# Optimization experiments

Hardware: AMD Instinct MI355X
Metric: run time of the kernel (lower is better)

The kernel has to match this reference:

```python
import jax, jax.numpy as jnp
import numpy as np

N_TOKENS = 65536   # number of embeddings to quantize
CODE_DIM = 768     # embedding dim
NUM_CODES = 4096   # codebook size


def setup_inputs() -> dict:
    key = jax.random.key(0)
    k1, k2 = jax.random.split(key)
    x = jax.random.normal(k1, (N_TOKENS, CODE_DIM), dtype=jnp.float32)
    codebook = jax.random.normal(k2, (NUM_CODES, CODE_DIM), dtype=jnp.float32)
    return {"x": x, "codebook": codebook}


def reference(x, codebook):
    # argmin over squared distances == argmin over cdist (sqrt is monotone).
    x2 = jnp.sum(x * x, axis=-1, keepdims=True)          # [N, 1]
    c2 = jnp.sum(codebook * codebook, axis=-1)           # [K]
    dist = x2 + c2[None, :] - 2.0 * jnp.einsum('nd,kd->nk', x, codebook)  # [N, K]
    indices = jnp.argmin(dist, axis=-1)                  # [N] int
    quantized = codebook[indices]                        # gather [N, D]
    # straight-through estimator: forward = quantized, grad flows to x
    q_ste = x + jax.lax.stop_gradient(quantized - x)
    return q_ste, indices
```

## Files before the change

kernel.cpp:

```cpp
#include <hip/hip_runtime.h>

#define N_TOKENS  65536
#define CODE_DIM  768
#define NUM_CODES 4096

#define MARGIN 0.006f
#define FLTMAX 3.4028235e38f

typedef __attribute__((ext_vector_type(8))) short bf16x8;
typedef __attribute__((ext_vector_type(4))) float f32x4;

__device__ __forceinline__ unsigned short f2bf(float f) {
  unsigned int u = __float_as_uint(f);
  unsigned int r = (u + 0x7fffu + ((u >> 16) & 1u)) >> 16;
  return (unsigned short)r;
}
__device__ __forceinline__ float bf2f(unsigned short h) {
  return __uint_as_float(((unsigned int)h) << 16);
}
__device__ __forceinline__ void gl2lds16(const void* g, void* l) {
  __builtin_amdgcn_global_load_lds(
      (const __attribute__((address_space(1))) unsigned int*)g,
      (__attribute__((address_space(3))) unsigned int*)l, 16, 0, 0);
}

__global__ __launch_bounds__(256) void vq_convert_kernel(
    const float* __restrict__ x, const float* __restrict__ cb,
    unsigned short* __restrict__ xh, unsigned short* __restrict__ xl,
    unsigned short* __restrict__ cbh, unsigned short* __restrict__ cbl,
    float* __restrict__ x2, float* __restrict__ c2, int* __restrict__ fcnt) {
  if (blockIdx.x == 0 && threadIdx.x == 0) *fcnt = 0;
  const int wave = threadIdx.x >> 6;
  const int lane = threadIdx.x & 63;
  const int row  = blockIdx.x * 4 + wave;
  const float* src;
  unsigned short *hdst, *ldst;
  float* ndst;
  if (row < N_TOKENS) {
    src = x + (size_t)row * CODE_DIM;
    hdst = xh + (size_t)row * CODE_DIM;
    ldst = xl + (size_t)row * CODE_DIM;
    ndst = x2 + row;
  } else {
    const int r = row - N_TOKENS;
    if (r >= NUM_CODES) return;
    src = cb + (size_t)r * CODE_DIM;
    hdst = cbh + (size_t)r * CODE_DIM;
    ldst = cbl + (size_t)r * CODE_DIM;
    ndst = c2 + r;
  }
  const float4* s4 = (const float4*)src;
  ushort4* h4 = (ushort4*)hdst;
  ushort4* l4 = (ushort4*)ldst;
  float acc = 0.f;
#pragma unroll
  for (int i = 0; i < 3; ++i) {
    float4 f = s4[lane + 64 * i];
    ushort4 h, l;
    h.x = f2bf(f.x); l.x = f2bf(f.x - bf2f(h.x));
    h.y = f2bf(f.y); l.y = f2bf(f.y - bf2f(h.y));
    h.z = f2bf(f.z); l.z = f2bf(f.z - bf2f(h.z));
    h.w = f2bf(f.w); l.w = f2bf(f.w - bf2f(h.w));
    h4[lane + 64 * i] = h;
    l4[lane + 64 * i] = l;
    acc += (f.x * f.x + f.y * f.y) + (f.z * f.z + f.w * f.w);
  }
#pragma unroll
  for (int off = 32; off > 0; off >>= 1) acc += __shfl_down(acc, off, 64);
  if (lane == 0) *ndst = acc;
}

#define BT 256
#define KTILE 256
#define NKT (NUM_CODES / KTILE)
#define NSTEP (CODE_DIM / 32)
#define TOTSTEP (NKT * NSTEP)

__global__ __launch_bounds__(512, 2) void vq_mfma_kernel(
    const unsigned short* __restrict__ xh, const unsigned short* __restrict__ xl,
    const unsigned short* __restrict__ cbh, const unsigned short* __restrict__ cbl,
    const float* __restrict__ c2, int* __restrict__ out_idx,
    int* __restrict__ fcnt, int* __restrict__ flist) {
  __shared__ __align__(16) unsigned short sA[2][BT * 64];
  __shared__ __align__(16) unsigned short sB[2][KTILE * 64];
  __shared__ float redv[512], redsv[512];
  __shared__ int   redi[512];

  const int tid = threadIdx.x;
  const int wave = tid >> 6, lane = tid & 63;
  const int l15 = lane & 15, quad = lane >> 4;
  const int wr = wave >> 1, wc = wave & 1;
  const int tokBase = blockIdx.x * BT;

  const int lr = lane >> 3;
  const int cc = (lane & 7) ^ lr;
  const int hsel = cc >> 2;
  const int coff = (cc & 3) * 8;
  const unsigned short* pAsrc = hsel ? xl : xh;
  const unsigned short* pBsrc = hsel ? cbl : cbh;
  const size_t aOff = (size_t)(tokBase + wave * 32 + lr) * CODE_DIM + coff;
  const size_t bOff = (size_t)(wave * 32 + lr) * CODE_DIM + coff;

  const int aposh = (quad ^ (l15 & 7)) * 8;
  const int aBaseH = (wr * 64 + l15) * 64 + aposh;
  const int aBaseL = (wr * 64 + l15) * 64 + (aposh ^ 32);
  const int bBaseH = (wc * 128 + l15) * 64 + aposh;
  const int bBaseL = (wc * 128 + l15) * 64 + (aposh ^ 32);

  float v[4][4], sv[4][4];
  int bi[4][4];
#pragma unroll
  for (int i = 0; i < 4; ++i)
#pragma unroll
    for (int r = 0; r < 4; ++r) { v[i][r] = FLTMAX; sv[i][r] = FLTMAX; bi[i][r] = 0; }

  auto STAGE = [&](int slot, int s) {
    const int sk0 = (s % NSTEP) * 32;
    const size_t sbb = (size_t)(s / NSTEP) * (KTILE * (size_t)CODE_DIM);
#pragma unroll
    for (int t = 0; t < 4; ++t)
      gl2lds16(pAsrc + aOff + (size_t)t * (8 * CODE_DIM) + sk0,
               &sA[slot][(wave * 32 + t * 8) * 64]);
#pragma unroll
    for (int t = 0; t < 4; ++t)
      gl2lds16(pBsrc + sbb + bOff + (size_t)t * (8 * CODE_DIM) + sk0,
               &sB[slot][(wave * 32 + t * 8) * 64]);
  };

  STAGE(0, 0);
  asm volatile("s_waitcnt vmcnt(0)" ::: "memory");
  __builtin_amdgcn_s_barrier();
  __builtin_amdgcn_sched_barrier(0);

  for (int kt = 0; kt < NKT; ++kt) {
    f32x4 acc[4][8];
#pragma unroll
    for (int i = 0; i < 4; ++i)
#pragma unroll
      for (int j = 0; j < 8; ++j) acc[i][j] = (f32x4){0.f, 0.f, 0.f, 0.f};

    for (int ksq = 0; ksq < NSTEP; ++ksq) {
      const int gstep = kt * NSTEP + ksq;
      const int cur = gstep & 1;
      const bool more = (gstep < TOTSTEP - 1);
      if (more) STAGE(cur ^ 1, gstep + 1);

      const unsigned short* As = sA[cur];
      const unsigned short* Bs = sB[cur];
      bf16x8 fah[4], fal[4];
#pragma unroll
      for (int i = 0; i < 4; ++i) {
        fah[i] = *(const bf16x8*)(As + aBaseH + i * 1024);
        fal[i] = *(const bf16x8*)(As + aBaseL + i * 1024);
      }
#pragma unroll
      for (int jp = 0; jp < 4; ++jp) {
        bf16x8 fbh[2], fbl[2];
#pragma unroll
        for (int jj = 0; jj < 2; ++jj) {
          const int j = jp * 2 + jj;
          fbh[jj] = *(const bf16x8*)(Bs + bBaseH + j * 1024);
          fbl[jj] = *(const bf16x8*)(Bs + bBaseL + j * 1024);
        }
        __builtin_amdgcn_s_setprio(1);
#pragma unroll
        for (int i = 0; i < 4; ++i)
#pragma unroll
          for (int jj = 0; jj < 2; ++jj) {
            const int j = jp * 2 + jj;
            acc[i][j] = __builtin_amdgcn_mfma_f32_16x16x32_bf16(fah[i], fbh[jj], acc[i][j], 0, 0, 0);
            acc[i][j] = __builtin_amdgcn_mfma_f32_16x16x32_bf16(fah[i], fbl[jj], acc[i][j], 0, 0, 0);
            acc[i][j] = __builtin_amdgcn_mfma_f32_16x16x32_bf16(fal[i], fbh[jj], acc[i][j], 0, 0, 0);
          }
        __builtin_amdgcn_s_setprio(0);
      }
      asm volatile("s_waitcnt vmcnt(0)" ::: "memory");
      __builtin_amdgcn_s_barrier();
      __builtin_amdgcn_sched_barrier(0);
    }

    const int kbase = kt * KTILE;
#pragma unroll
    for (int j = 0; j < 8; ++j) {
      const int kcol = kbase + wc * 128 + j * 16 + l15;
      const float c2j = c2[kcol];
#pragma unroll
      for (int i = 0; i < 4; ++i)
#pragma unroll
        for (int r = 0; r < 4; ++r) {
          float s = fmaf(-2.0f, acc[i][j][r], c2j);
          float vo = v[i][r];
          sv[i][r] = fminf(sv[i][r], fmaxf(s, vo));
          bool lt = s < vo;
          v[i][r]  = lt ? s : vo;
          bi[i][r] = lt ? kcol : bi[i][r];
        }
    }
  }

#pragma unroll
  for (int i = 0; i < 4; ++i)
#pragma unroll
    for (int r = 0; r < 4; ++r) {
      float vv = v[i][r], svv = sv[i][r];
      int ii = bi[i][r];
#pragma unroll
      for (int m = 1; m < 16; m <<= 1) {
        float ov = __shfl_xor(vv, m, 64);
        float osv = __shfl_xor(svv, m, 64);
        int oi = __shfl_xor(ii, m, 64);
        float nsv = fminf(fminf(svv, osv), fmaxf(vv, ov));
        bool take = (ov < vv) || (ov == vv && oi < ii);
        vv = take ? ov : vv;
        ii = take ? oi : ii;
        svv = nsv;
      }
      if (l15 == 0) {
        int row = wr * 64 + i * 16 + quad * 4 + r;
        redv[row * 2 + wc] = vv;
        redsv[row * 2 + wc] = svv;
        redi[row * 2 + wc] = ii;
      }
    }
  __syncthreads();
  if (tid < 256) {
    float v0 = redv[tid * 2], v1 = redv[tid * 2 + 1];
    float s0 = redsv[tid * 2], s1 = redsv[tid * 2 + 1];
    int i0 = redi[tid * 2], i1 = redi[tid * 2 + 1];
    bool take = (v1 < v0) || (v1 == v0 && i1 < i0);
    float bv = take ? v1 : v0;
    int bidx = take ? i1 : i0;
    float bsv = fminf(fminf(s0, s1), fmaxf(v0, v1));
    out_idx[tokBase + tid] = bidx;
    if (bsv - bv < MARGIN) {
      int p = atomicAdd(fcnt, 1);
      flist[p] = tokBase + tid;
    }
  }
}

__global__ __launch_bounds__(256) void vq_rescan_kernel(
    const float* __restrict__ x, const float* __restrict__ cb,
    const float* __restrict__ x2, const float* __restrict__ c2,
    const int* __restrict__ fcnt, const int* __restrict__ flist,
    int* __restrict__ out_idx) {
  __shared__ float xs[4][CODE_DIM];
  __shared__ float rv[256];
  __shared__ int ri[256];
  const int nf = *fcnt;
  const int ngr = (nf + 3) >> 2;
  for (int g = blockIdx.x; g < ngr; g += gridDim.x) {
    const int base = g * 4;
    int tok[4];
#pragma unroll
    for (int t = 0; t < 4; ++t) tok[t] = flist[min(base + t, nf - 1)];
    __syncthreads();
    if (threadIdx.x < 192) {
#pragma unroll
      for (int t = 0; t < 4; ++t)
        ((float4*)xs[t])[threadIdx.x] =
            ((const float4*)(x + (size_t)tok[t] * CODE_DIM))[threadIdx.x];
    }
    __syncthreads();
    float bv[4]; int bidx[4];
#pragma unroll
    for (int t = 0; t < 4; ++t) { bv[t] = FLTMAX; bidx[t] = 0; }
    for (int kk = 0; kk < NUM_CODES / 256; ++kk) {
      const int k = kk * 256 + threadIdx.x;
      const float4* crow = (const float4*)(cb + (size_t)k * CODE_DIM);
      float a0 = 0.f, a1 = 0.f, a2 = 0.f, a3 = 0.f;
      for (int c = 0; c < CODE_DIM / 4; ++c) {
        float4 cv = crow[c];
        float4 x0 = ((float4*)xs[0])[c];
        float4 x1 = ((float4*)xs[1])[c];
        float4 x2v = ((float4*)xs[2])[c];
        float4 x3 = ((float4*)xs[3])[c];
        a0 += (x0.x * cv.x + x0.y * cv.y) + (x0.z * cv.z + x0.w * cv.w);
        a1 += (x1.x * cv.x + x1.y * cv.y) + (x1.z * cv.z + x1.w * cv.w);
        a2 += (x2v.x * cv.x + x2v.y * cv.y) + (x2v.z * cv.z + x2v.w * cv.w);
        a3 += (x3.x * cv.x + x3.y * cv.y) + (x3.z * cv.z + x3.w * cv.w);
      }
      const float c2k = c2[k];
      float d0 = (x2[tok[0]] + c2k) - 2.0f * a0;
      float d1 = (x2[tok[1]] + c2k) - 2.0f * a1;
      float d2 = (x2[tok[2]] + c2k) - 2.0f * a2;
      float d3 = (x2[tok[3]] + c2k) - 2.0f * a3;
      if (d0 < bv[0]) { bv[0] = d0; bidx[0] = k; }
      if (d1 < bv[1]) { bv[1] = d1; bidx[1] = k; }
      if (d2 < bv[2]) { bv[2] = d2; bidx[2] = k; }
      if (d3 < bv[3]) { bv[3] = d3; bidx[3] = k; }
    }
#pragma unroll
    for (int t = 0; t < 4; ++t) {
      __syncthreads();
      rv[threadIdx.x] = bv[t];
      ri[threadIdx.x] = bidx[t];
      __syncthreads();
      for (int s = 128; s > 0; s >>= 1) {
        if (threadIdx.x < s) {
          float ov = rv[threadIdx.x + s];
          int oi = ri[threadIdx.x + s];
          if (ov < rv[threadIdx.x] ||
              (ov == rv[threadIdx.x] && oi < ri[threadIdx.x])) {
            rv[threadIdx.x] = ov;
            ri[threadIdx.x] = oi;
          }
        }
        __syncthreads();
      }
      if (threadIdx.x == 0 && base + t < nf) out_idx[tok[t]] = ri[0];
    }
  }
}

__global__ __launch_bounds__(256) void vq_gather_kernel(
    const float* __restrict__ cb, const int* __restrict__ idx,
    float* __restrict__ out) {
  const int wave = threadIdx.x >> 6;
  const int lane = threadIdx.x & 63;
  const int token = blockIdx.x * 4 + wave;
  const int k = idx[token];
  const float4* src = (const float4*)(cb + (size_t)k * CODE_DIM);
  float4* dst = (float4*)(out + (size_t)token * CODE_DIM);
#pragma unroll
  for (int i = 0; i < 3; ++i) dst[lane + 64 * i] = src[lane + 64 * i];
  if (lane == 0) out[(size_t)N_TOKENS * CODE_DIM + token] = (float)k;
}

#define MT 64
#define KT 128
#define DT 32
#define LDSTRIDE 36

__global__ __launch_bounds__(256) void vq_norms_kernel(
    const float* __restrict__ x, const float* __restrict__ cb,
    float* __restrict__ x2, float* __restrict__ c2) {
  const int wave = threadIdx.x >> 6;
  const int lane = threadIdx.x & 63;
  const int row = blockIdx.x * 4 + wave;
  const float* src;
  float* dst;
  if (row < N_TOKENS) {
    src = x + (size_t)row * CODE_DIM;
    dst = x2 + row;
  } else {
    const int r = row - N_TOKENS;
    if (r >= NUM_CODES) return;
    src = cb + (size_t)r * CODE_DIM;
    dst = c2 + r;
  }
  const float4* s4 = (const float4*)src;
  float acc = 0.f;
#pragma unroll
  for (int i = 0; i < 3; ++i) {
    float4 vv = s4[lane + 64 * i];
    acc += (vv.x * vv.x + vv.y * vv.y) + (vv.z * vv.z + vv.w * vv.w);
  }
#pragma unroll
  for (int off = 32; off > 0; off >>= 1) acc += __shfl_down(acc, off, 64);
  if (lane == 0) *dst = acc;
}

__global__ __launch_bounds__(256) void vq_argmin_kernel(
    const float* __restrict__ x, const float* __restrict__ cb,
    const float* __restrict__ x2, const float* __restrict__ c2,
    int* __restrict__ out_idx) {
  __shared__ float xs[MT * LDSTRIDE];
  __shared__ float cs[KT * LDSTRIDE];
  __shared__ float x2s[MT];
  __shared__ float c2s[KT];
  const int tid = threadIdx.x;
  const int tx = tid & 15;
  const int ty = tid >> 4;
  const int tokBase = blockIdx.x * MT;
  if (tid < MT) x2s[tid] = x2[tokBase + tid];
  float bestv[4];
  int besti[4];
#pragma unroll
  for (int i = 0; i < 4; ++i) { bestv[i] = FLTMAX; besti[i] = 0; }
  const float4* xg = (const float4*)x;
  const float4* cg = (const float4*)cb;
  for (int kt = 0; kt < NUM_CODES / KT; ++kt) {
    const int kBase = kt * KT;
    __syncthreads();
    if (tid < KT) c2s[tid] = c2[kBase + tid];
    float acc[4][8];
#pragma unroll
    for (int i = 0; i < 4; ++i)
#pragma unroll
      for (int j = 0; j < 8; ++j) acc[i][j] = 0.f;
    for (int dc = 0; dc < CODE_DIM / DT; ++dc) {
      __syncthreads();
#pragma unroll
      for (int r = 0; r < 2; ++r) {
        int fidx = tid + 256 * r;
        int row = fidx >> 3, c4 = fidx & 7;
        float4 vv = xg[(size_t)(tokBase + row) * (CODE_DIM / 4) + dc * 8 + c4];
        *(float4*)&xs[row * LDSTRIDE + c4 * 4] = vv;
      }
#pragma unroll
      for (int r = 0; r < 4; ++r) {
        int fidx = tid + 256 * r;
        int row = fidx >> 3, c4 = fidx & 7;
        float4 vv = cg[(size_t)(kBase + row) * (CODE_DIM / 4) + dc * 8 + c4];
        *(float4*)&cs[row * LDSTRIDE + c4 * 4] = vv;
      }
      __syncthreads();
#pragma unroll
      for (int dd = 0; dd < DT / 4; ++dd) {
        float4 xv[4], cv[8];
#pragma unroll
        for (int i = 0; i < 4; ++i)
          xv[i] = *(const float4*)&xs[(ty + 16 * i) * LDSTRIDE + dd * 4];
#pragma unroll
        for (int j = 0; j < 8; ++j)
          cv[j] = *(const float4*)&cs[(tx + 16 * j) * LDSTRIDE + dd * 4];
#pragma unroll
        for (int i = 0; i < 4; ++i)
#pragma unroll
          for (int j = 0; j < 8; ++j)
            acc[i][j] += (xv[i].x * cv[j].x + xv[i].y * cv[j].y) +
                         (xv[i].z * cv[j].z + xv[i].w * cv[j].w);
      }
    }
#pragma unroll
    for (int i = 0; i < 4; ++i) {
      const float xx = x2s[ty + 16 * i];
#pragma unroll
      for (int j = 0; j < 8; ++j) {
        float dist = (xx + c2s[tx + 16 * j]) - 2.0f * acc[i][j];
        int k = kBase + tx + 16 * j;
        if (dist < bestv[i]) { bestv[i] = dist; besti[i] = k; }
      }
    }
  }
  __syncthreads();
  float* rdv = xs;
  int* rdi = (int*)cs;
#pragma unroll
  for (int i = 0; i < 4; ++i) {
    const int m = ty + 16 * i;
    rdv[m * 16 + tx] = bestv[i];
    rdi[m * 16 + tx] = besti[i];
  }
  __syncthreads();
  if (tid < MT) {
    float bv = rdv[tid * 16];
    int bidx = rdi[tid * 16];
#pragma unroll
    for (int t = 1; t < 16; ++t) {
      float vv = rdv[tid * 16 + t];
      int kk = rdi[tid * 16 + t];
      if (vv < bv || (vv == bv && kk < bidx)) { bv = vv; bidx = kk; }
    }
    out_idx[tokBase + tid] = bidx;
  }
}

extern "C" void kernel_launch(void* const* d_in, const int* in_sizes, int n_in,
                              void* d_out, int out_size, void* d_ws, size_t ws_size,
                              hipStream_t stream) {
  (void)in_sizes; (void)n_in; (void)out_size;
  const float* x = (const float*)d_in[0];
  const float* cb = (const float*)d_in[1];
  float* out = (float*)d_out;

  char* w = (char*)d_ws;
  unsigned short* xh = (unsigned short*)w;  w += (size_t)N_TOKENS * CODE_DIM * 2;
  unsigned short* xl = (unsigned short*)w;  w += (size_t)N_TOKENS * CODE_DIM * 2;
  unsigned short* cbh = (unsigned short*)w; w += (size_t)NUM_CODES * CODE_DIM * 2;
  unsigned short* cbl = (unsigned short*)w; w += (size_t)NUM_CODES * CODE_DIM * 2;
  float* x2 = (float*)w;  w += (size_t)N_TOKENS * 4;
  float* c2 = (float*)w;  w += (size_t)NUM_CODES * 4;
  int* idx = (int*)w;     w += (size_t)N_TOKENS * 4;
  int* flist = (int*)w;   w += (size_t)N_TOKENS * 4;
  int* fcnt = (int*)w;    w += 256;
  const size_t need = (size_t)(w - (char*)d_ws);

  if (ws_size >= need) {
    vq_convert_kernel<<<(N_TOKENS + NUM_CODES) / 4, 256, 0, stream>>>(
        x, cb, xh, xl, cbh, cbl, x2, c2, fcnt);
    vq_mfma_kernel<<<N_TOKENS / BT, 512, 0, stream>>>(
        xh, xl, cbh, cbl, c2, idx, fcnt, flist);
    vq_rescan_kernel<<<512, 256, 0, stream>>>(x, cb, x2, c2, fcnt, flist, idx);
    vq_gather_kernel<<<N_TOKENS / 4, 256, 0, stream>>>(cb, idx, out);
  } else {
    float* fx2 = (float*)d_ws;
    float* fc2 = fx2 + N_TOKENS;
    int* fidx = (int*)(fc2 + NUM_CODES);
    vq_norms_kernel<<<(N_TOKENS + NUM_CODES + 3) / 4, 256, 0, stream>>>(x, cb, fx2, fc2);
    vq_argmin_kernel<<<N_TOKENS / MT, 256, 0, stream>>>(x, cb, fx2, fc2, fidx);
    vq_gather_kernel<<<N_TOKENS / 4, 256, 0, stream>>>(cb, fidx, out);
  }
}
```

Measured before the change: 1.818 ms.

## Fuse codebook gather into MFMA kernel and split staging around MFMA phases

The separate gather kernel is removed. The MFMA kernel now writes the quantized rows and float indices for its own tokens at the end, and the rescan kernel rewrites the rows for flagged tokens with the corrected index. The inner loop is also reordered into three MFMA phases (hi*hi, hi*lo, lo*hi), and the A and B global-to-LDS prefetches are issued between phases instead of together at the start. This saves one kernel launch and a full pass re-reading the index array, and aims for better overlap of loads with MFMA, at the cost of more live B fragment registers (fbh and fbl, 8 each).

```diff
diff --git a/kernel.cpp b/kernel.cpp
--- a/kernel.cpp
+++ b/kernel.cpp
@@ -79,12 +79,14 @@
 __global__ __launch_bounds__(512, 2) void vq_mfma_kernel(
     const unsigned short* __restrict__ xh, const unsigned short* __restrict__ xl,
     const unsigned short* __restrict__ cbh, const unsigned short* __restrict__ cbl,
-    const float* __restrict__ c2, int* __restrict__ out_idx,
+    const float* __restrict__ c2, const float* __restrict__ cb,
+    float* __restrict__ out, int* __restrict__ out_idx,
     int* __restrict__ fcnt, int* __restrict__ flist) {
   __shared__ __align__(16) unsigned short sA[2][BT * 64];
   __shared__ __align__(16) unsigned short sB[2][KTILE * 64];
   __shared__ float redv[512], redsv[512];
   __shared__ int   redi[512];
+  __shared__ int   sIdx[256];
 
   const int tid = threadIdx.x;
   const int wave = tid >> 6, lane = tid & 63;
@@ -114,20 +116,16 @@
 #pragma unroll
     for (int r = 0; r < 4; ++r) { v[i][r] = FLTMAX; sv[i][r] = FLTMAX; bi[i][r] = 0; }
 
-  auto STAGE = [&](int slot, int s) {
-    const int sk0 = (s % NSTEP) * 32;
-    const size_t sbb = (size_t)(s / NSTEP) * (KTILE * (size_t)CODE_DIM);
+  {
 #pragma unroll
     for (int t = 0; t < 4; ++t)
-      gl2lds16(pAsrc + aOff + (size_t)t * (8 * CODE_DIM) + sk0,
-               &sA[slot][(wave * 32 + t * 8) * 64]);
+      gl2lds16(pAsrc + aOff + (size_t)t * (8 * CODE_DIM),
+               &sA[0][(wave * 32 + t * 8) * 64]);
 #pragma unroll
     for (int t = 0; t < 4; ++t)
-      gl2lds16(pBsrc + sbb + bOff + (size_t)t * (8 * CODE_DIM) + sk0,
-               &sB[slot][(wave * 32 + t * 8) * 64]);
-  };
-
-  STAGE(0, 0);
+      gl2lds16(pBsrc + bOff + (size_t)t * (8 * CODE_DIM),
+               &sB[0][(wave * 32 + t * 8) * 64]);
+  }
   asm volatile("s_waitcnt vmcnt(0)" ::: "memory");
   __builtin_amdgcn_s_barrier();
   __builtin_amdgcn_sched_barrier(0);
@@ -143,37 +141,59 @@
       const int gstep = kt * NSTEP + ksq;
       const int cur = gstep & 1;
       const bool more = (gstep < TOTSTEP - 1);
-      if (more) STAGE(cur ^ 1, gstep + 1);
-
+      const int ns = gstep + 1;
+      const int nk0 = (ns % NSTEP) * 32;
+      const size_t nbb = (size_t)(ns / NSTEP) * (KTILE * (size_t)CODE_DIM);
       const unsigned short* As = sA[cur];
       const unsigned short* Bs = sB[cur];
-      bf16x8 fah[4], fal[4];
-#pragma unroll
-      for (int i = 0; i < 4; ++i) {
-        fah[i] = *(const bf16x8*)(As + aBaseH + i * 1024);
-        fal[i] = *(const bf16x8*)(As + aBaseL + i * 1024);
-      }
-#pragma unroll
-      for (int jp = 0; jp < 4; ++jp) {
-        bf16x8 fbh[2], fbl[2];
-#pragma unroll
-        for (int jj = 0; jj < 2; ++jj) {
-          const int j = jp * 2 + jj;
-          fbh[jj] = *(const bf16x8*)(Bs + bBaseH + j * 1024);
-          fbl[jj] = *(const bf16x8*)(Bs + bBaseL + j * 1024);
-        }
-        __builtin_amdgcn_s_setprio(1);
-#pragma unroll
-        for (int i = 0; i < 4; ++i)
-#pragma unroll
-          for (int jj = 0; jj < 2; ++jj) {
-            const int j = jp * 2 + jj;
-            acc[i][j] = __builtin_amdgcn_mfma_f32_16x16x32_bf16(fah[i], fbh[jj], acc[i][j], 0, 0, 0);
-            acc[i][j] = __builtin_amdgcn_mfma_f32_16x16x32_bf16(fah[i], fbl[jj], acc[i][j], 0, 0, 0);
-            acc[i][j] = __builtin_amdgcn_mfma_f32_16x16x32_bf16(fal[i], fbh[jj], acc[i][j], 0, 0, 0);
-          }
-        __builtin_amdgcn_s_setprio(0);
-      }
+
+      if (more) {
+#pragma unroll
+        for (int t = 0; t < 4; ++t)
+          gl2lds16(pAsrc + aOff + (size_t)t * (8 * CODE_DIM) + nk0,
+                   &sA[cur ^ 1][(wave * 32 + t * 8) * 64]);
+      }
+
+      bf16x8 fah[4], fal[4], fbh[8], fbl[8];
+#pragma unroll
+      for (int i = 0; i < 4; ++i) fah[i] = *(const bf16x8*)(As + aBaseH + i * 1024);
+#pragma unroll
+      for (int j = 0; j < 8; ++j) fbh[j] = *(const bf16x8*)(Bs + bBaseH + j * 1024);
+      __builtin_amdgcn_s_setprio(1);
+#pragma unroll
+      for (int i = 0; i < 4; ++i)
+#pragma unroll
+        for (int j = 0; j < 8; ++j)
+          acc[i][j] = __builtin_amdgcn_mfma_f32_16x16x32_bf16(fah[i], fbh[j], acc[i][j], 0, 0, 0);
+      __builtin_amdgcn_s_setprio(0);
+
+      if (more) {
+#pragma unroll
+        for (int t = 0; t < 4; ++t)
+          gl2lds16(pBsrc + nbb + bOff + (size_t)t * (8 * CODE_DIM) + nk0,
+                   &sB[cur ^ 1][(wave * 32 + t * 8) * 64]);
+      }
+
+#pragma unroll
+      for (int j = 0; j < 8; ++j) fbl[j] = *(const bf16x8*)(Bs + bBaseL + j * 1024);
+      __builtin_amdgcn_s_setprio(1);
+#pragma unroll
+      for (int i = 0; i < 4; ++i)
+#pragma unroll
+        for (int j = 0; j < 8; ++j)
+          acc[i][j] = __builtin_amdgcn_mfma_f32_16x16x32_bf16(fah[i], fbl[j], acc[i][j], 0, 0, 0);
+      __builtin_amdgcn_s_setprio(0);
+
+#pragma unroll
+      for (int i = 0; i < 4; ++i) fal[i] = *(const bf16x8*)(As + aBaseL + i * 1024);
+      __builtin_amdgcn_s_setprio(1);
+#pragma unroll
+      for (int i = 0; i < 4; ++i)
+#pragma unroll
+        for (int j = 0; j < 8; ++j)
+          acc[i][j] = __builtin_amdgcn_mfma_f32_16x16x32_bf16(fal[i], fbh[j], acc[i][j], 0, 0, 0);
+      __builtin_amdgcn_s_setprio(0);
+
       asm volatile("s_waitcnt vmcnt(0)" ::: "memory");
       __builtin_amdgcn_s_barrier();
       __builtin_amdgcn_sched_barrier(0);
@@ -232,18 +252,30 @@
     int bidx = take ? i1 : i0;
     float bsv = fminf(fminf(s0, s1), fmaxf(v0, v1));
     out_idx[tokBase + tid] = bidx;
+    sIdx[tid] = bidx;
     if (bsv - bv < MARGIN) {
       int p = atomicAdd(fcnt, 1);
       flist[p] = tokBase + tid;
     }
   }
+  __syncthreads();
+  for (int tt = 0; tt < 32; ++tt) {
+    const int t = wave * 32 + tt;
+    const int k = sIdx[t];
+    const float4* src = (const float4*)(cb + (size_t)k * CODE_DIM);
+    float4* dst = (float4*)(out + (size_t)(tokBase + t) * CODE_DIM);
+#pragma unroll
+    for (int i2 = 0; i2 < 3; ++i2) dst[lane + 64 * i2] = src[lane + 64 * i2];
+  }
+  if (tid < 256)
+    out[(size_t)N_TOKENS * CODE_DIM + tokBase + tid] = (float)sIdx[tid];
 }
 
 __global__ __launch_bounds__(256) void vq_rescan_kernel(
     const float* __restrict__ x, const float* __restrict__ cb,
     const float* __restrict__ x2, const float* __restrict__ c2,
     const int* __restrict__ fcnt, const int* __restrict__ flist,
-    int* __restrict__ out_idx) {
+    int* __restrict__ out_idx, float* __restrict__ out) {
   __shared__ float xs[4][CODE_DIM];
   __shared__ float rv[256];
   __shared__ int ri[256];
@@ -308,7 +340,16 @@
         }
         __syncthreads();
       }
-      if (threadIdx.x == 0 && base + t < nf) out_idx[tok[t]] = ri[0];
+      const int kfix = ri[0];
+      if (base + t < nf) {
+        if (threadIdx.x < 192)
+          ((float4*)(out + (size_t)tok[t] * CODE_DIM))[threadIdx.x] =
+              ((const float4*)(cb + (size_t)kfix * CODE_DIM))[threadIdx.x];
+        if (threadIdx.x == 0) {
+          out_idx[tok[t]] = kfix;
+          out[(size_t)N_TOKENS * CODE_DIM + tok[t]] = (float)kfix;
+        }
+      }
     }
   }
 }
@@ -481,9 +522,8 @@
     vq_convert_kernel<<<(N_TOKENS + NUM_CODES) / 4, 256, 0, stream>>>(
         x, cb, xh, xl, cbh, cbl, x2, c2, fcnt);
     vq_mfma_kernel<<<N_TOKENS / BT, 512, 0, stream>>>(
-        xh, xl, cbh, cbl, c2, idx, fcnt, flist);
-    vq_rescan_kernel<<<512, 256, 0, stream>>>(x, cb, x2, c2, fcnt, flist, idx);
-    vq_gather_kernel<<<N_TOKENS / 4, 256, 0, stream>>>(cb, idx, out);
+        xh, xl, cbh, cbl, c2, cb, out, idx, fcnt, flist);
+    vq_rescan_kernel<<<512, 256, 0, stream>>>(x, cb, x2, c2, fcnt, flist, idx, out);
   } else {
     float* fx2 = (float*)d_ws;
     float* fc2 = fx2 + N_TOKENS;
```

Result: slower. 1.934 ms (+6.4%).

## Replace split-bf16 three-pass MFMA with single fp16 MFMA and wider rescan margin

Applied to the files above, without the earlier changes.

Replaces the bf16 hi/lo split (three MFMAs per tile, which emulates fp32) with a single fp16 conversion and one f16 MFMA per K chunk. Each LDS stage now carries 64 K-elements, which cuts both the matrix-core work and the global traffic for the converted operands. Because fp16 is less precise, the ambiguity margin grows from 0.006 to 0.12, so more tokens fall back to the exact fp32 rescan. The rescan kernel is widened to handle 8 tokens per group to absorb that larger fallback list. The risk is that rescan cost grows sharply, and the fixed margin may not cover the fp16 error on every input.

```diff
diff --git a/kernel.cpp b/kernel.cpp
--- a/kernel.cpp
+++ b/kernel.cpp
@@ -4,19 +4,15 @@
 #define CODE_DIM  768
 #define NUM_CODES 4096
 
-#define MARGIN 0.006f
+#define MARGIN 0.12f
 #define FLTMAX 3.4028235e38f
 
-typedef __attribute__((ext_vector_type(8))) short bf16x8;
+typedef __attribute__((ext_vector_type(8))) _Float16 f16x8;
 typedef __attribute__((ext_vector_type(4))) float f32x4;
 
-__device__ __forceinline__ unsigned short f2bf(float f) {
-  unsigned int u = __float_as_uint(f);
-  unsigned int r = (u + 0x7fffu + ((u >> 16) & 1u)) >> 16;
-  return (unsigned short)r;
-}
-__device__ __forceinline__ float bf2f(unsigned short h) {
-  return __uint_as_float(((unsigned int)h) << 16);
+__device__ __forceinline__ unsigned short f2h(float f) {
+  _Float16 h = (_Float16)f;
+  return *(unsigned short*)&h;
 }
 __device__ __forceinline__ void gl2lds16(const void* g, void* l) {
   __builtin_amdgcn_global_load_lds(
@@ -26,43 +22,35 @@
 
 __global__ __launch_bounds__(256) void vq_convert_kernel(
     const float* __restrict__ x, const float* __restrict__ cb,
-    unsigned short* __restrict__ xh, unsigned short* __restrict__ xl,
-    unsigned short* __restrict__ cbh, unsigned short* __restrict__ cbl,
+    unsigned short* __restrict__ xh, unsigned short* __restrict__ ch,
     float* __restrict__ x2, float* __restrict__ c2, int* __restrict__ fcnt) {
   if (blockIdx.x == 0 && threadIdx.x == 0) *fcnt = 0;
   const int wave = threadIdx.x >> 6;
   const int lane = threadIdx.x & 63;
   const int row  = blockIdx.x * 4 + wave;
   const float* src;
-  unsigned short *hdst, *ldst;
+  unsigned short* hdst;
   float* ndst;
   if (row < N_TOKENS) {
     src = x + (size_t)row * CODE_DIM;
     hdst = xh + (size_t)row * CODE_DIM;
-    ldst = xl + (size_t)row * CODE_DIM;
     ndst = x2 + row;
   } else {
     const int r = row - N_TOKENS;
     if (r >= NUM_CODES) return;
     src = cb + (size_t)r * CODE_DIM;
-    hdst = cbh + (size_t)r * CODE_DIM;
-    ldst = cbl + (size_t)r * CODE_DIM;
+    hdst = ch + (size_t)r * CODE_DIM;
     ndst = c2 + r;
   }
   const float4* s4 = (const float4*)src;
   ushort4* h4 = (ushort4*)hdst;
-  ushort4* l4 = (ushort4*)ldst;
   float acc = 0.f;
 #pragma unroll
   for (int i = 0; i < 3; ++i) {
     float4 f = s4[lane + 64 * i];
-    ushort4 h, l;
-    h.x = f2bf(f.x); l.x = f2bf(f.x - bf2f(h.x));
-    h.y = f2bf(f.y); l.y = f2bf(f.y - bf2f(h.y));
-    h.z = f2bf(f.z); l.z = f2bf(f.z - bf2f(h.z));
-    h.w = f2bf(f.w); l.w = f2bf(f.w - bf2f(h.w));
+    ushort4 h;
+    h.x = f2h(f.x); h.y = f2h(f.y); h.z = f2h(f.z); h.w = f2h(f.w);
     h4[lane + 64 * i] = h;
-    l4[lane + 64 * i] = l;
     acc += (f.x * f.x + f.y * f.y) + (f.z * f.z + f.w * f.w);
   }
 #pragma unroll
@@ -73,12 +61,11 @@
 #define BT 256
 #define KTILE 256
 #define NKT (NUM_CODES / KTILE)
-#define NSTEP (CODE_DIM / 32)
-#define TOTSTEP (NKT * NSTEP)
+#define NST (CODE_DIM / 64)
+#define TOT (NKT * NST)
 
 __global__ __launch_bounds__(512, 2) void vq_mfma_kernel(
-    const unsigned short* __restrict__ xh, const unsigned short* __restrict__ xl,
-    const unsigned short* __restrict__ cbh, const unsigned short* __restrict__ cbl,
+    const unsigned short* __restrict__ xh, const unsigned short* __restrict__ ch,
     const float* __restrict__ c2, int* __restrict__ out_idx,
     int* __restrict__ fcnt, int* __restrict__ flist) {
   __shared__ __align__(16) unsigned short sA[2][BT * 64];
@@ -93,19 +80,15 @@
   const int tokBase = blockIdx.x * BT;
 
   const int lr = lane >> 3;
-  const int cc = (lane & 7) ^ lr;
-  const int hsel = cc >> 2;
-  const int coff = (cc & 3) * 8;
-  const unsigned short* pAsrc = hsel ? xl : xh;
-  const unsigned short* pBsrc = hsel ? cbl : cbh;
-  const size_t aOff = (size_t)(tokBase + wave * 32 + lr) * CODE_DIM + coff;
-  const size_t bOff = (size_t)(wave * 32 + lr) * CODE_DIM + coff;
-
-  const int aposh = (quad ^ (l15 & 7)) * 8;
-  const int aBaseH = (wr * 64 + l15) * 64 + aposh;
-  const int aBaseL = (wr * 64 + l15) * 64 + (aposh ^ 32);
-  const int bBaseH = (wc * 128 + l15) * 64 + aposh;
-  const int bBaseL = (wc * 128 + l15) * 64 + (aposh ^ 32);
+  const int cSrc = (lane & 7) ^ lr;
+  const size_t aOff = (size_t)(tokBase + wave * 32 + lr) * CODE_DIM + cSrc * 8;
+  const size_t bOff = (size_t)(wave * 32 + lr) * CODE_DIM + cSrc * 8;
+
+  const int apos = (quad ^ (l15 & 7)) * 8;
+  const int aB0 = (wr * 64 + l15) * 64 + apos;
+  const int aB1 = (wr * 64 + l15) * 64 + (apos ^ 32);
+  const int bB0 = (wc * 128 + l15) * 64 + apos;
+  const int bB1 = (wc * 128 + l15) * 64 + (apos ^ 32);
 
   float v[4][4], sv[4][4];
   int bi[4][4];
@@ -115,15 +98,15 @@
     for (int r = 0; r < 4; ++r) { v[i][r] = FLTMAX; sv[i][r] = FLTMAX; bi[i][r] = 0; }
 
   auto STAGE = [&](int slot, int s) {
-    const int sk0 = (s % NSTEP) * 32;
-    const size_t sbb = (size_t)(s / NSTEP) * (KTILE * (size_t)CODE_DIM);
+    const int kw = (s % NST) * 64;
+    const size_t rb = (size_t)(s / NST) * (KTILE * (size_t)CODE_DIM);
 #pragma unroll
     for (int t = 0; t < 4; ++t)
-      gl2lds16(pAsrc + aOff + (size_t)t * (8 * CODE_DIM) + sk0,
+      gl2lds16(xh + aOff + (size_t)t * (8 * CODE_DIM) + kw,
                &sA[slot][(wave * 32 + t * 8) * 64]);
 #pragma unroll
     for (int t = 0; t < 4; ++t)
-      gl2lds16(pBsrc + sbb + bOff + (size_t)t * (8 * CODE_DIM) + sk0,
+      gl2lds16(ch + rb + bOff + (size_t)t * (8 * CODE_DIM) + kw,
                &sB[slot][(wave * 32 + t * 8) * 64]);
   };
 
@@ -139,41 +122,37 @@
 #pragma unroll
       for (int j = 0; j < 8; ++j) acc[i][j] = (f32x4){0.f, 0.f, 0.f, 0.f};
 
-    for (int ksq = 0; ksq < NSTEP; ++ksq) {
-      const int gstep = kt * NSTEP + ksq;
+    for (int ks = 0; ks < NST; ++ks) {
+      const int gstep = kt * NST + ks;
       const int cur = gstep & 1;
-      const bool more = (gstep < TOTSTEP - 1);
-      if (more) STAGE(cur ^ 1, gstep + 1);
-
       const unsigned short* As = sA[cur];
       const unsigned short* Bs = sB[cur];
-      bf16x8 fah[4], fal[4];
-#pragma unroll
-      for (int i = 0; i < 4; ++i) {
-        fah[i] = *(const bf16x8*)(As + aBaseH + i * 1024);
-        fal[i] = *(const bf16x8*)(As + aBaseL + i * 1024);
-      }
-#pragma unroll
-      for (int jp = 0; jp < 4; ++jp) {
-        bf16x8 fbh[2], fbl[2];
-#pragma unroll
-        for (int jj = 0; jj < 2; ++jj) {
-          const int j = jp * 2 + jj;
-          fbh[jj] = *(const bf16x8*)(Bs + bBaseH + j * 1024);
-          fbl[jj] = *(const bf16x8*)(Bs + bBaseL + j * 1024);
-        }
-        __builtin_amdgcn_s_setprio(1);
-#pragma unroll
-        for (int i = 0; i < 4; ++i)
-#pragma unroll
-          for (int jj = 0; jj < 2; ++jj) {
-            const int j = jp * 2 + jj;
-            acc[i][j] = __builtin_amdgcn_mfma_f32_16x16x32_bf16(fah[i], fbh[jj], acc[i][j], 0, 0, 0);
-            acc[i][j] = __builtin_amdgcn_mfma_f32_16x16x32_bf16(fah[i], fbl[jj], acc[i][j], 0, 0, 0);
-            acc[i][j] = __builtin_amdgcn_mfma_f32_16x16x32_bf16(fal[i], fbh[jj], acc[i][j], 0, 0, 0);
-          }
-        __builtin_amdgcn_s_setprio(0);
-      }
+      if (gstep < TOT - 1) STAGE(cur ^ 1, gstep + 1);
+
+      f16x8 fa[4], fb[8];
+#pragma unroll
+      for (int i = 0; i < 4; ++i) fa[i] = *(const f16x8*)(As + aB0 + i * 1024);
+#pragma unroll
+      for (int j = 0; j < 8; ++j) fb[j] = *(const f16x8*)(Bs + bB0 + j * 1024);
+      __builtin_amdgcn_s_setprio(1);
+#pragma unroll
+      for (int i = 0; i < 4; ++i)
+#pragma unroll
+        for (int j = 0; j < 8; ++j)
+          acc[i][j] = __builtin_amdgcn_mfma_f32_16x16x32_f16(fa[i], fb[j], acc[i][j], 0, 0, 0);
+      __builtin_amdgcn_s_setprio(0);
+#pragma unroll
+      for (int i = 0; i < 4; ++i) fa[i] = *(const f16x8*)(As + aB1 + i * 1024);
+#pragma unroll
+      for (int j = 0; j < 8; ++j) fb[j] = *(const f16x8*)(Bs + bB1 + j * 1024);
+      __builtin_amdgcn_s_setprio(1);
+#pragma unroll
+      for (int i = 0; i < 4; ++i)
+#pragma unroll
+        for (int j = 0; j < 8; ++j)
+          acc[i][j] = __builtin_amdgcn_mfma_f32_16x16x32_f16(fa[i], fb[j], acc[i][j], 0, 0, 0);
+      __builtin_amdgcn_s_setprio(0);
+
       asm volatile("s_waitcnt vmcnt(0)" ::: "memory");
       __builtin_amdgcn_s_barrier();
       __builtin_amdgcn_sched_barrier(0);
@@ -244,54 +223,50 @@
     const float* __restrict__ x2, const float* __restrict__ c2,
     const int* __restrict__ fcnt, const int* __restrict__ flist,
     int* __restrict__ out_idx) {
-  __shared__ float xs[4][CODE_DIM];
+  __shared__ float xs[8][CODE_DIM];
   __shared__ float rv[256];
   __shared__ int ri[256];
   const int nf = *fcnt;
-  const int ngr = (nf + 3) >> 2;
+  const int ngr = (nf + 7) >> 3;
   for (int g = blockIdx.x; g < ngr; g += gridDim.x) {
-    const int base = g * 4;
-    int tok[4];
-#pragma unroll
-    for (int t = 0; t < 4; ++t) tok[t] = flist[min(base + t, nf - 1)];
+    const int base = g * 8;
+    int tok[8];
+#pragma unroll
+    for (int t = 0; t < 8; ++t) tok[t] = flist[min(base + t, nf - 1)];
     __syncthreads();
     if (threadIdx.x < 192) {
 #pragma unroll
-      for (int t = 0; t < 4; ++t)
+      for (int t = 0; t < 8; ++t)
         ((float4*)xs[t])[threadIdx.x] =
             ((const float4*)(x + (size_t)tok[t] * CODE_DIM))[threadIdx.x];
     }
     __syncthreads();
-    float bv[4]; int bidx[4];
-#pragma unroll
-    for (int t = 0; t < 4; ++t) { bv[t] = FLTMAX; bidx[t] = 0; }
+    float bv[8]; int bidx[8];
+#pragma unroll
+    for (int t = 0; t < 8; ++t) { bv[t] = FLTMAX; bidx[t] = 0; }
     for (int kk = 0; kk < NUM_CODES / 256; ++kk) {
       const int k = kk * 256 + threadIdx.x;
       const float4* crow = (const float4*)(cb + (size_t)k * CODE_DIM);
-      float a0 = 0.f, a1 = 0.f, a2 = 0.f, a3 = 0.f;
+      float a[8];
+#pragma unroll
+      for (int t = 0; t < 8; ++t) a[t] = 0.f;
       for (int c = 0; c < CODE_DIM / 4; ++c) {
         float4 cv = crow[c];
-        float4 x0 = ((float4*)xs[0])[c];
-        float4 x1 = ((float4*)xs[1])[c];
-        float4 x2v = ((float4*)xs[2])[c];
-        float4 x3 = ((float4*)xs[3])[c];
-        a0 += (x0.x * cv.x + x0.y * cv.y) + (x0.z * cv.z + x0.w * cv.w);
-        a1 += (x1.x * cv.x + x1.y * cv.y) + (x1.z * cv.z + x1.w * cv.w);
-        a2 += (x2v.x * cv.x + x2v.y * cv.y) + (x2v.z * cv.z + x2v.w * cv.w);
-        a3 += (x3.x * cv.x + x3.y * cv.y) + (x3.z * cv.z + x3.w * cv.w);
+#pragma unroll
+        for (int t = 0; t < 8; ++t) {
+          float4 xv = ((float4*)xs[t])[c];
+          a[t] += (xv.x * cv.x + xv.y * cv.y) + (xv.z * cv.z + xv.w * cv.w);
+        }
       }
       const float c2k = c2[k];
-      float d0 = (x2[tok[0]] + c2k) - 2.0f * a0;
-      float d1 = (x2[tok[1]] + c2k) - 2.0f * a1;
-      float d2 = (x2[tok[2]] + c2k) - 2.0f * a2;
-      float d3 = (x2[tok[3]] + c2k) - 2.0f * a3;
-      if (d0 < bv[0]) { bv[0] = d0; bidx[0] = k; }
-      if (d1 < bv[1]) { bv[1] = d1; bidx[1] = k; }
-      if (d2 < bv[2]) { bv[2] = d2; bidx[2] = k; }
-      if (d3 < bv[3]) { bv[3] = d3; bidx[3] = k; }
-    }
-#pragma unroll
-    for (int t = 0; t < 4; ++t) {
+#pragma unroll
+      for (int t = 0; t < 8; ++t) {
+        float d = (x2[tok[t]] + c2k) - 2.0f * a[t];
+        if (d < bv[t]) { bv[t] = d; bidx[t] = k; }
+      }
+    }
+#pragma unroll
+    for (int t = 0; t < 8; ++t) {
       __syncthreads();
       rv[threadIdx.x] = bv[t];
       ri[threadIdx.x] = bidx[t];
@@ -467,9 +442,7 @@
 
   char* w = (char*)d_ws;
   unsigned short* xh = (unsigned short*)w;  w += (size_t)N_TOKENS * CODE_DIM * 2;
-  unsigned short* xl = (unsigned short*)w;  w += (size_t)N_TOKENS * CODE_DIM * 2;
-  unsigned short* cbh = (unsigned short*)w; w += (size_t)NUM_CODES * CODE_DIM * 2;
-  unsigned short* cbl = (unsigned short*)w; w += (size_t)NUM_CODES * CODE_DIM * 2;
+  unsigned short* ch = (unsigned short*)w;  w += (size_t)NUM_CODES * CODE_DIM * 2;
   float* x2 = (float*)w;  w += (size_t)N_TOKENS * 4;
   float* c2 = (float*)w;  w += (size_t)NUM_CODES * 4;
   int* idx = (int*)w;     w += (size_t)N_TOKENS * 4;
@@ -479,9 +452,9 @@
 
   if (ws_size >= need) {
     vq_convert_kernel<<<(N_TOKENS + NUM_CODES) / 4, 256, 0, stream>>>(
-        x, cb, xh, xl, cbh, cbl, x2, c2, fcnt);
+        x, cb, xh, ch, x2, c2, fcnt);
     vq_mfma_kernel<<<N_TOKENS / BT, 512, 0, stream>>>(
-        xh, xl, cbh, cbl, c2, idx, fcnt, flist);
+        xh, ch, c2, idx, fcnt, flist);
     vq_rescan_kernel<<<512, 256, 0, stream>>>(x, cb, x2, c2, fcnt, flist, idx);
     vq_gather_kernel<<<N_TOKENS / 4, 256, 0, stream>>>(cb, idx, out);
   } else {
```

New measurement: 1.728 ms. 1.05x faster.
